# Kernel optimization log

Hardware: AMD Instinct MI355X
Metric: run time of the kernel (lower is better)

Reference implementation:

```python
import jax, jax.numpy as jnp
import numpy as np

N = 50000      # nodes
E = 800000     # edges
F_IN = 256     # num_n_feature
EMB = 128      # emb_size
GF = 32        # num_g_feature
G = 256        # graphs in batch
NEG_SLOPE = 0.2


def setup_inputs() -> dict:
    key = jax.random.key(0)
    ks = jax.random.split(key, 20)
    p = lambda i, shape: (jax.random.normal(ks[i], shape, jnp.float32) * 0.05)
    return {
        "x": jax.random.normal(ks[0], (N, F_IN), jnp.float32),
        "edges_idx": jax.random.randint(ks[1], (2, E), 0, N, dtype=jnp.int32),
        "batch_idx": jnp.sort(jax.random.randint(ks[2], (N,), 0, G, dtype=jnp.int32)),
        "g_features": jax.random.normal(ks[3], (G, GF), jnp.float32),
        # GATConv 1
        "W1": p(4, (F_IN, EMB)), "a1_src": p(5, (EMB,)), "a1_dst": p(6, (EMB,)), "b1": p(7, (EMB,)),
        # GATConv 2
        "W2": p(8, (EMB, EMB)), "a2_src": p(9, (EMB,)), "a2_dst": p(10, (EMB,)), "b2": p(11, (EMB,)),
        # lin_g
        "Wg": p(12, (GF, EMB)), "bg": p(13, (EMB,)),
        # out head: Linear(3*emb, 2)
        "Wo": p(14, (3 * EMB, 2)), "bo": p(15, (2,)),
    }


def gat_conv(x, src, dst, W, a_src, a_dst, b, n):
    """PyG GATConv, heads=1, with self-loops; attention dropout omitted (eval)."""
    h = x @ W                                  # [N, emb]
    loop = jnp.arange(n, dtype=src.dtype)
    src = jnp.concatenate([src, loop])         # add self loops
    dst = jnp.concatenate([dst, loop])
    e = jax.nn.leaky_relu((h @ a_src)[src] + (h @ a_dst)[dst], NEG_SLOPE)  # [E+N]
    # segment softmax over destination nodes
    m = jax.lax.stop_gradient(jax.ops.segment_max(e, dst, num_segments=n))
    m = jnp.where(jnp.isfinite(m), m, 0.0)
    p = jnp.exp(e - m[dst])
    den = jax.ops.segment_sum(p, dst, num_segments=n)
    alpha = p / den[dst]
    out = jax.ops.segment_sum(alpha[:, None] * h[src], dst, num_segments=n)
    return out + b


def reference(x, edges_idx, batch_idx, g_features,
              W1, a1_src, a1_dst, b1, W2, a2_src, a2_dst, b2,
              Wg, bg, Wo, bo):
    src, dst = edges_idx[0], edges_idx[1]
    h = gat_conv(x, src, dst, W1, a1_src, a1_dst, b1, N)
    h = gat_conv(h, src, dst, W2, a2_src, a2_dst, b2, N)
    # global mean / max pooling per graph
    counts = jax.ops.segment_sum(jnp.ones((N,), h.dtype), batch_idx, num_segments=G)
    mean = jax.ops.segment_sum(h, batch_idx, num_segments=G) / jnp.maximum(counts, 1.0)[:, None]
    mx = jax.ops.segment_max(h, batch_idx, num_segments=G)
    mx = jnp.where(jnp.isfinite(mx), mx, 0.0)
    g_ft = g_features @ Wg + bg
    flat = jnp.concatenate([mean, mx, g_ft], axis=1)   # [G, 3*emb]
    return jax.nn.log_softmax(flat @ Wo + bo, axis=-1)  # [G, 2]
```

## Files before the change

### kernel.cpp

```cpp
#include <hip/hip_runtime.h>
#include <hip/hip_bf16.h>

#define N_NODES 50000
#define N_EDGES 800000
#define FIN 256
#define EMB 128
#define NGRAPH 256
#define TOT_E (N_EDGES + N_NODES)
#define NP 98
#define RBLK 196
#define NB 391

typedef __bf16 bf16;
typedef __attribute__((ext_vector_type(8))) __bf16 bf16x8;
typedef __attribute__((ext_vector_type(4))) __bf16 bf16x4;
typedef __attribute__((ext_vector_type(2))) __bf16 bf16x2;
typedef __attribute__((ext_vector_type(4))) float f32x4;
typedef __attribute__((ext_vector_type(4))) int i32x4;

__global__ void transpose2_kernel(const float* __restrict__ W1, bf16* __restrict__ WT1,
                                  const float* __restrict__ W2, bf16* __restrict__ WT2) {
    int t = blockIdx.x * 256 + threadIdx.x;
    if (t < FIN * EMB) {
        int c = t / FIN, r = t - c * FIN;
        WT1[t] = (bf16)W1[r * EMB + c];
    } else if (t < FIN * EMB + EMB * EMB) {
        int u = t - FIN * EMB;
        int c = u / EMB, r = u - c * EMB;
        WT2[u] = (bf16)W2[r * EMB + c];
    }
}

__global__ __launch_bounds__(256)
void hist_part_kernel(const int* __restrict__ e_dst, int* __restrict__ counts,
                      int* __restrict__ mat) {
    __shared__ int lh[NP];
    int t = threadIdx.x;
    for (int k = t; k < NP; k += 256) lh[k] = 0;
    __syncthreads();
    const int NQ = N_EDGES / 4;
    int base = blockIdx.x * 1024;
#pragma unroll
    for (int j = 0; j < 4; ++j) {
        int i = base + j * 256 + t;
        if (i < NQ) {
            i32x4 d4 = *(const i32x4*)(e_dst + 4 * i);
#pragma unroll
            for (int k = 0; k < 4; ++k) {
                atomicAdd(&counts[d4[k]], 1);
                atomicAdd(&lh[d4[k] >> 9], 1);
            }
        }
    }
    __syncthreads();
    for (int k = t; k < NP; k += 256) mat[k * RBLK + blockIdx.x] = lh[k];
}

__global__ __launch_bounds__(1024)
void scan_block_kernel(const int* __restrict__ counts, int* __restrict__ offsets,
                       int* __restrict__ blocksums) {
    __shared__ int lds[1024];
    int t = threadIdx.x;
    int idx = blockIdx.x * 1024 + t;
    int v = (idx < N_NODES) ? counts[idx] + 1 : 0;
    lds[t] = v;
    __syncthreads();
    for (int d = 1; d < 1024; d <<= 1) {
        int u = (t >= d) ? lds[t - d] : 0;
        __syncthreads();
        lds[t] += u;
        __syncthreads();
    }
    if (idx < N_NODES) offsets[idx] = lds[t] - v;
    if (t == 1023) blocksums[blockIdx.x] = lds[1023];
}

__global__ __launch_bounds__(1024)
void scan_fix_kernel(int* __restrict__ offsets, const int* __restrict__ blocksums,
                     int nblk, int* __restrict__ sorted) {
    __shared__ int sprefix;
    int t = threadIdx.x, b = blockIdx.x;
    if (t < 64) {
        int v = (t < b && t < nblk) ? blocksums[t] : 0;
#pragma unroll
        for (int mk = 32; mk >= 1; mk >>= 1) v += __shfl_xor(v, mk);
        if (t == 0) sprefix = v;
    }
    __syncthreads();
    int idx = b * 1024 + t;
    if (idx < N_NODES) {
        int off = offsets[idx] + sprefix;
        offsets[idx] = off;
        sorted[off] = idx;
    }
    if (idx == 0) offsets[N_NODES] = TOT_E;
}

__global__ __launch_bounds__(256)
void rowscan_kernel(int* __restrict__ mat, int* __restrict__ rowsum) {
    __shared__ int lds[256];
    int p = blockIdx.x, t = threadIdx.x;
    int v = (t < RBLK) ? mat[p * RBLK + t] : 0;
    lds[t] = v;
    __syncthreads();
    for (int d = 1; d < 256; d <<= 1) {
        int u = (t >= d) ? lds[t - d] : 0;
        __syncthreads();
        lds[t] += u;
        __syncthreads();
    }
    if (t < RBLK) mat[p * RBLK + t] = lds[t] - v;
    if (t == 255) rowsum[p] = lds[255];
}

__global__ __launch_bounds__(128)
void partbase_kernel(const int* __restrict__ rowsum, int* __restrict__ poff) {
    __shared__ int lds[128];
    int t = threadIdx.x;
    int v = (t < NP) ? rowsum[t] : 0;
    lds[t] = v;
    __syncthreads();
    for (int d = 1; d < 128; d <<= 1) {
        int u = (t >= d) ? lds[t - d] : 0;
        __syncthreads();
        lds[t] += u;
        __syncthreads();
    }
    if (t < NP) poff[t] = lds[t] - v;
    if (t == 0) poff[NP] = N_EDGES;
}

__global__ __launch_bounds__(256)
void radix_scatter_kernel(const int* __restrict__ e_src, const int* __restrict__ e_dst,
                          const int* __restrict__ mat, const int* __restrict__ poff,
                          unsigned* __restrict__ pairs) {
    __shared__ int cur[NP];
    int t = threadIdx.x;
    for (int k = t; k < NP; k += 256) cur[k] = poff[k] + mat[k * RBLK + blockIdx.x];
    __syncthreads();
    const int NQ = N_EDGES / 4;
    int base = blockIdx.x * 1024;
#pragma unroll
    for (int j = 0; j < 4; ++j) {
        int i = base + j * 256 + t;
        if (i < NQ) {
            i32x4 d4 = *(const i32x4*)(e_dst + 4 * i);
            i32x4 s4 = *(const i32x4*)(e_src + 4 * i);
#pragma unroll
            for (int k = 0; k < 4; ++k) {
                int d = d4[k];
                int pos = atomicAdd(&cur[d >> 9], 1);
                pairs[pos] = ((unsigned)d << 16) | (unsigned)s4[k];
            }
        }
    }
}

__global__ __launch_bounds__(1024)
void bucket_place_kernel(const int* __restrict__ poff, const int* __restrict__ offsets,
                         const unsigned* __restrict__ pairs, int* __restrict__ sorted) {
    int b = blockIdx.x;
    int t = threadIdx.x;
    int lo = b * 128;
    __shared__ int cur[128];
    if (t < 128 && lo + t < N_NODES) cur[t] = offsets[lo + t] + 1;
    __syncthreads();
    int p = b >> 2;
    int p0 = poff[p], p1 = poff[p + 1];
    unsigned blo = (unsigned)b;
    for (int i = p0 + t; i < p1; i += 1024) {
        unsigned v = pairs[i];
        unsigned d = v >> 16;
        if ((d >> 7) == blo) {
            int pos = atomicAdd(&cur[d & 127], 1);
            sorted[pos] = (int)(v & 0xFFFFu);
        }
    }
}

template<int K, typename AT>
__global__ __launch_bounds__(256)
void gemm_kernel(const AT* __restrict__ A, const bf16* __restrict__ WT,
                 bf16* __restrict__ C, int M,
                 const float* __restrict__ a_src, const float* __restrict__ a_dst,
                 float* __restrict__ s_src, float* __restrict__ s_dst) {
    __shared__ __align__(16) bf16 As[32][64];
    __shared__ __align__(16) bf16 Bs[128][64];
    __shared__ float sbuf[2][32];
    int tid = threadIdx.x;
    int wave = tid >> 6, lane = tid & 63;
    int rowHalf = wave & 1, colHalf = wave >> 1;
    int m0 = blockIdx.x * 32;

    f32x4 acc[4];
#pragma unroll
    for (int i = 0; i < 4; ++i) acc[i] = (f32x4){0.f, 0.f, 0.f, 0.f};

    for (int k0 = 0; k0 < K; k0 += 64) {
        if constexpr (sizeof(AT) == 4) {
#pragma unroll
            for (int it = 0; it < 2; ++it) {
                int task = tid + it * 256;
                int row = task >> 4, seg4 = task & 15;
                int gr = m0 + row;
                float4 f = make_float4(0.f, 0.f, 0.f, 0.f);
                if (gr < M) f = *(const float4*)((const float*)A + (size_t)gr * K + k0 + seg4 * 4);
                bf16x4 b4 = (bf16x4){(bf16)f.x, (bf16)f.y, (bf16)f.z, (bf16)f.w};
                int slot = seg4 >> 1, half8 = seg4 & 1;
                int ss = slot ^ (row & 7);
                *(bf16x4*)(&As[row][ss * 8 + half8 * 4]) = b4;
            }
        } else {
            int row = tid >> 3, slot = tid & 7;
            int gr = m0 + row;
            uint4 v = make_uint4(0u, 0u, 0u, 0u);
            if (gr < M) v = *(const uint4*)((const bf16*)A + (size_t)gr * K + k0 + slot * 8);
            int ss = slot ^ (row & 7);
            *(uint4*)(&As[row][ss * 8]) = v;
        }
#pragma unroll
        for (int it = 0; it < 4; ++it) {
            int task = tid + it * 256;
            int col = task >> 3, slot = task & 7;
            uint4 v = *(const uint4*)(WT + (size_t)col * K + k0 + slot * 8);
            int ss = slot ^ (col & 7);
            *(uint4*)(&Bs[col][ss * 8]) = v;
        }
        __syncthreads();
        int tr = rowHalf * 16 + (lane & 15);
        int kseg = lane >> 4;
        bf16x8 af0 = *(const bf16x8*)(&As[tr][((kseg) ^ (tr & 7)) * 8]);
        bf16x8 af1 = *(const bf16x8*)(&As[tr][((4 + kseg) ^ (tr & 7)) * 8]);
#pragma unroll
        for (int n = 0; n < 4; ++n) {
            int c = colHalf * 64 + n * 16 + (lane & 15);
            bf16x8 b0 = *(const bf16x8*)(&Bs[c][((kseg) ^ (c & 7)) * 8]);
            bf16x8 b1 = *(const bf16x8*)(&Bs[c][((4 + kseg) ^ (c & 7)) * 8]);
            acc[n] = __builtin_amdgcn_mfma_f32_16x16x32_bf16(af0, b0, acc[n], 0, 0, 0);
            acc[n] = __builtin_amdgcn_mfma_f32_16x16x32_bf16(af1, b1, acc[n], 0, 0, 0);
        }
        __syncthreads();
    }
    int rbase = m0 + rowHalf * 16 + ((lane >> 4) << 2);
    int cb = lane & 15;
#pragma unroll
    for (int n = 0; n < 4; ++n) {
        int col = colHalf * 64 + n * 16 + cb;
#pragma unroll
        for (int rr = 0; rr < 4; ++rr) {
            int row = rbase + rr;
            if (row < M) C[(size_t)row * 128 + col] = (bf16)acc[n][rr];
        }
    }
    if (tid < 64) sbuf[tid >> 5][tid & 31] = 0.f;
    __syncthreads();
    float a_s[4], a_d[4];
#pragma unroll
    for (int n = 0; n < 4; ++n) {
        a_s[n] = a_src[colHalf * 64 + n * 16 + cb];
        a_d[n] = a_dst[colHalf * 64 + n * 16 + cb];
    }
#pragma unroll
    for (int rr = 0; rr < 4; ++rr) {
        float ps = 0.f, pd = 0.f;
#pragma unroll
        for (int n = 0; n < 4; ++n) {
            ps += acc[n][rr] * a_s[n];
            pd += acc[n][rr] * a_d[n];
        }
#pragma unroll
        for (int mk = 8; mk >= 1; mk >>= 1) {
            ps += __shfl_xor(ps, mk);
            pd += __shfl_xor(pd, mk);
        }
        if (cb == 0) {
            int tr16 = rowHalf * 16 + (lane >> 4) * 4 + rr;
            atomicAdd(&sbuf[0][tr16], ps);
            atomicAdd(&sbuf[1][tr16], pd);
        }
    }
    __syncthreads();
    if (tid < 32 && m0 + tid < M) {
        s_src[m0 + tid] = sbuf[0][tid];
        s_dst[m0 + tid] = sbuf[1][tid];
    }
}

template<typename OUT_T>
__global__ __launch_bounds__(256)
void agg_kernel(const int* __restrict__ offsets, const int* __restrict__ sorted_src,
                const float* __restrict__ s_src, const float* __restrict__ s_dst,
                const bf16* __restrict__ h, const float* __restrict__ bias,
                OUT_T* __restrict__ out) {
    int tid = threadIdx.x;
    int wave = tid >> 6, lane = tid & 63;
    int gl = lane & 15;
    int gbase = lane & 48;
    int d = blockIdx.x * 16 + wave * 4 + (lane >> 4);
    if (d >= N_NODES) return;
    int r0 = offsets[d];
    int deg = offsets[d + 1] - r0;
    float sd = s_dst[d];

    int sv0 = 0, sv1 = 0;
    float ev0 = -INFINITY, ev1 = -INFINITY;
    if (gl < deg) {
        sv0 = sorted_src[r0 + gl];
        float e = s_src[sv0] + sd;
        ev0 = (e > 0.f) ? e : 0.2f * e;
    }
    if (16 + gl < deg) {
        sv1 = sorted_src[r0 + 16 + gl];
        float e = s_src[sv1] + sd;
        ev1 = (e > 0.f) ? e : 0.2f * e;
    }
    float m = fmaxf(ev0, ev1);
    for (int i = 32 + gl; i < deg; i += 16) {
        int s = sorted_src[r0 + i];
        float e = s_src[s] + sd;
        e = (e > 0.f) ? e : 0.2f * e;
        m = fmaxf(m, e);
    }
#pragma unroll
    for (int mk = 8; mk >= 1; mk >>= 1) m = fmaxf(m, __shfl_xor(m, mk));

    float pv0 = (gl < deg) ? __expf(ev0 - m) : 0.f;
    float pv1 = (16 + gl < deg) ? __expf(ev1 - m) : 0.f;
    float den = pv0 + pv1;
    for (int i = 32 + gl; i < deg; i += 16) {
        int s = sorted_src[r0 + i];
        float e = s_src[s] + sd;
        e = (e > 0.f) ? e : 0.2f * e;
        den += __expf(e - m);
    }
#pragma unroll
    for (int mk = 8; mk >= 1; mk >>= 1) den += __shfl_xor(den, mk);

    float acc[8];
#pragma unroll
    for (int k = 0; k < 8; ++k) acc[k] = 0.f;

    int jm = (deg < 32) ? deg : 32;
#pragma unroll 8
    for (int j = 0; j < jm; ++j) {
        int src_lane = gbase + (j & 15);
        int s = __shfl((j < 16) ? sv0 : sv1, src_lane);
        float p = __shfl((j < 16) ? pv0 : pv1, src_lane);
        bf16x8 hv = *(const bf16x8*)(h + (size_t)s * 128 + gl * 8);
#pragma unroll
        for (int k = 0; k < 8; ++k) acc[k] += p * (float)hv[k];
    }
    for (int i = 32; i < deg; ++i) {
        int s = sorted_src[r0 + i];
        float e = s_src[s] + sd;
        e = (e > 0.f) ? e : 0.2f * e;
        float p = __expf(e - m);
        bf16x8 hv = *(const bf16x8*)(h + (size_t)s * 128 + gl * 8);
#pragma unroll
        for (int k = 0; k < 8; ++k) acc[k] += p * (float)hv[k];
    }

    float inv = 1.f / den;
    float4 bv0 = *(const float4*)(bias + gl * 8);
    float4 bv1 = *(const float4*)(bias + gl * 8 + 4);
    float o[8] = {acc[0] * inv + bv0.x, acc[1] * inv + bv0.y,
                  acc[2] * inv + bv0.z, acc[3] * inv + bv0.w,
                  acc[4] * inv + bv1.x, acc[5] * inv + bv1.y,
                  acc[6] * inv + bv1.z, acc[7] * inv + bv1.w};
    if constexpr (sizeof(OUT_T) == 2) {
        bf16x8 ov;
#pragma unroll
        for (int k = 0; k < 8; ++k) ov[k] = (bf16)o[k];
        *(bf16x8*)((bf16*)out + (size_t)d * 128 + gl * 8) = ov;
    } else {
        float* op = (float*)out + (size_t)d * 128 + gl * 8;
        *(float4*)op       = (float4){o[0], o[1], o[2], o[3]};
        *(float4*)(op + 4) = (float4){o[4], o[5], o[6], o[7]};
    }
}

__global__ __launch_bounds__(256)
void pool_kernel(const bf16* __restrict__ out2, const int* __restrict__ batch_idx,
                 float* __restrict__ mean, float* __restrict__ mx) {
    int g = blockIdx.x;
    int j = threadIdx.x & 127;
    int grp = threadIdx.x >> 7;
    int lo = 0, hi = N_NODES;
    while (lo < hi) { int mid = (lo + hi) >> 1; if (batch_idx[mid] < g) lo = mid + 1; else hi = mid; }
    int start = lo;
    hi = N_NODES;
    while (lo < hi) { int mid = (lo + hi) >> 1; if (batch_idx[mid] < g + 1) lo = mid + 1; else hi = mid; }
    int end = lo;

    float s = 0.f, mmax = -INFINITY;
    for (int r = start + grp; r < end; r += 2) {
        float v = (float)out2[(size_t)r * 128 + j];
        s += v;
        mmax = fmaxf(mmax, v);
    }
    __shared__ float ls[2][128], lm[2][128];
    ls[grp][j] = s; lm[grp][j] = mmax;
    __syncthreads();
    if (grp == 0) {
        int cnt = end - start;
        float sum = ls[0][j] + ls[1][j];
        float mv = fmaxf(lm[0][j], lm[1][j]);
        mean[g * 128 + j] = sum / fmaxf((float)cnt, 1.f);
        mx[g * 128 + j] = (cnt > 0) ? mv : 0.f;
    }
}

__global__ __launch_bounds__(128)
void head_kernel(const float* __restrict__ mean, const float* __restrict__ mx,
                 const float* __restrict__ gfeat, const float* __restrict__ Wg,
                 const float* __restrict__ bg, const float* __restrict__ Wo,
                 const float* __restrict__ bo, float* __restrict__ out) {
    int g = blockIdx.x;
    int j = threadIdx.x;
    float gft = bg[j];
#pragma unroll
    for (int k = 0; k < 32; ++k)
        gft += gfeat[g * 32 + k] * Wg[k * 128 + j];
    float mj = mean[g * 128 + j], xj = mx[g * 128 + j];
    float p0 = mj * Wo[j * 2 + 0] + xj * Wo[(128 + j) * 2 + 0] + gft * Wo[(256 + j) * 2 + 0];
    float p1 = mj * Wo[j * 2 + 1] + xj * Wo[(128 + j) * 2 + 1] + gft * Wo[(256 + j) * 2 + 1];
#pragma unroll
    for (int m = 32; m >= 1; m >>= 1) { p0 += __shfl_xor(p0, m); p1 += __shfl_xor(p1, m); }
    __shared__ float l0s[2], l1s[2];
    int wv = j >> 6;
    if ((j & 63) == 0) { l0s[wv] = p0; l1s[wv] = p1; }
    __syncthreads();
    if (j == 0) {
        float l0 = l0s[0] + l0s[1] + bo[0];
        float l1 = l1s[0] + l1s[1] + bo[1];
        float mm = fmaxf(l0, l1);
        float lse = mm + logf(__expf(l0 - mm) + __expf(l1 - mm));
        out[g * 2 + 0] = l0 - lse;
        out[g * 2 + 1] = l1 - lse;
    }
}

extern "C" void kernel_launch(void* const* d_in, const int* in_sizes, int n_in,
                              void* d_out, int out_size, void* d_ws, size_t ws_size,
                              hipStream_t stream) {
    const float* x     = (const float*)d_in[0];
    const int*   edges = (const int*)d_in[1];
    const int*   batch = (const int*)d_in[2];
    const float* gfeat = (const float*)d_in[3];
    const float* W1    = (const float*)d_in[4];
    const float* a1s   = (const float*)d_in[5];
    const float* a1d   = (const float*)d_in[6];
    const float* b1    = (const float*)d_in[7];
    const float* W2    = (const float*)d_in[8];
    const float* a2s   = (const float*)d_in[9];
    const float* a2d   = (const float*)d_in[10];
    const float* b2    = (const float*)d_in[11];
    const float* Wg    = (const float*)d_in[12];
    const float* bg    = (const float*)d_in[13];
    const float* Wo    = (const float*)d_in[14];
    const float* bo    = (const float*)d_in[15];

    char* ws = (char*)d_ws;
    bf16*     WT1       = (bf16*)(ws + 0);
    bf16*     WT2       = (bf16*)(ws + 65536);
    float*    s_src     = (float*)(ws + 98304);
    float*    s_dst     = (float*)(ws + 299008);
    int*      counts    = (int*)(ws + 499712);
    int*      blocksums = (int*)(ws + 700416);
    int*      mat       = (int*)(ws + 700672);
    int*      rowsum    = (int*)(ws + 777536);
    int*      poff      = (int*)(ws + 777984);
    int*      offsets   = (int*)(ws + 778432);
    int*      sorted    = (int*)(ws + 979136);
    bf16*     h         = (bf16*)(ws + 4502528);
    bf16*     out1      = (bf16*)(ws + 17302528);
    bf16*     out2      = (bf16*)(ws + 30102528);
    unsigned* pairs     = (unsigned*)(ws + 43002528);
    float*    pmean     = (float*)(ws + 55702528);
    float*    pmax      = (float*)(ws + 55833600);

    const int* e_src = edges;
    const int* e_dst = edges + N_EDGES;

    transpose2_kernel<<<(FIN * EMB + EMB * EMB + 255) / 256, 256, 0, stream>>>(W1, WT1, W2, WT2);

    hipMemsetAsync(counts, 0, N_NODES * sizeof(int), stream);
    hist_part_kernel<<<RBLK, 256, 0, stream>>>(e_dst, counts, mat);
    int nblk = (N_NODES + 1023) / 1024;
    scan_block_kernel<<<nblk, 1024, 0, stream>>>(counts, offsets, blocksums);
    scan_fix_kernel<<<nblk, 1024, 0, stream>>>(offsets, blocksums, nblk, sorted);
    rowscan_kernel<<<NP, 256, 0, stream>>>(mat, rowsum);
    partbase_kernel<<<1, 128, 0, stream>>>(rowsum, poff);
    radix_scatter_kernel<<<RBLK, 256, 0, stream>>>(e_src, e_dst, mat, poff, pairs);
    bucket_place_kernel<<<NB, 1024, 0, stream>>>(poff, offsets, pairs, sorted);

    int gemm_blocks = (N_NODES + 31) / 32;
    int agg_blocks = (N_NODES + 15) / 16;

    gemm_kernel<FIN, float><<<gemm_blocks, 256, 0, stream>>>(x, WT1, h, N_NODES,
                                                             a1s, a1d, s_src, s_dst);
    agg_kernel<bf16><<<agg_blocks, 256, 0, stream>>>(offsets, sorted, s_src, s_dst, h, b1, out1);

    gemm_kernel<EMB, bf16><<<gemm_blocks, 256, 0, stream>>>(out1, WT2, h, N_NODES,
                                                            a2s, a2d, s_src, s_dst);
    agg_kernel<bf16><<<agg_blocks, 256, 0, stream>>>(offsets, sorted, s_src, s_dst, h, b2, out2);

    pool_kernel<<<NGRAPH, 256, 0, stream>>>(out2, batch, pmean, pmax);
    head_kernel<<<NGRAPH, 128, 0, stream>>>(pmean, pmax, gfeat, Wg, bg, Wo, bo, (float*)d_out);
}
```

Baseline: 213.9 us.

## Fuse per-node counting and offset scan into per-partition CSR build kernel

Removes the global per-node atomic histogram, the memset and the two-pass global scan. Per-node counts and offsets are now computed inside each 512-node partition in LDS, then placed directly. The partition base is derived from poff plus nbase to account for the self-loop slots. This drops three launches and 800K global atomics, but uses only 98 blocks for the final placement instead of 391, so less parallelism.

```diff
diff --git a/kernel.cpp b/kernel.cpp
--- a/kernel.cpp
+++ b/kernel.cpp
@@ -9,7 +9,6 @@
 #define TOT_E (N_EDGES + N_NODES)
 #define NP 98
 #define RBLK 196
-#define NB 391
 
 typedef __bf16 bf16;
 typedef __attribute__((ext_vector_type(8))) __bf16 bf16x8;
@@ -31,9 +30,9 @@
     }
 }
 
-__global__ __launch_bounds__(256)
-void hist_part_kernel(const int* __restrict__ e_dst, int* __restrict__ counts,
-                      int* __restrict__ mat) {
+
+__global__ __launch_bounds__(256)
+void hist_part_kernel(const int* __restrict__ e_dst, int* __restrict__ mat) {
     __shared__ int lh[NP];
     int t = threadIdx.x;
     for (int k = t; k < NP; k += 256) lh[k] = 0;
@@ -46,54 +45,11 @@
         if (i < NQ) {
             i32x4 d4 = *(const i32x4*)(e_dst + 4 * i);
 #pragma unroll
-            for (int k = 0; k < 4; ++k) {
-                atomicAdd(&counts[d4[k]], 1);
-                atomicAdd(&lh[d4[k] >> 9], 1);
-            }
+            for (int k = 0; k < 4; ++k) atomicAdd(&lh[d4[k] >> 9], 1);
         }
     }
     __syncthreads();
     for (int k = t; k < NP; k += 256) mat[k * RBLK + blockIdx.x] = lh[k];
-}
-
-__global__ __launch_bounds__(1024)
-void scan_block_kernel(const int* __restrict__ counts, int* __restrict__ offsets,
-                       int* __restrict__ blocksums) {
-    __shared__ int lds[1024];
-    int t = threadIdx.x;
-    int idx = blockIdx.x * 1024 + t;
-    int v = (idx < N_NODES) ? counts[idx] + 1 : 0;
-    lds[t] = v;
-    __syncthreads();
-    for (int d = 1; d < 1024; d <<= 1) {
-        int u = (t >= d) ? lds[t - d] : 0;
-        __syncthreads();
-        lds[t] += u;
-        __syncthreads();
-    }
-    if (idx < N_NODES) offsets[idx] = lds[t] - v;
-    if (t == 1023) blocksums[blockIdx.x] = lds[1023];
-}
-
-__global__ __launch_bounds__(1024)
-void scan_fix_kernel(int* __restrict__ offsets, const int* __restrict__ blocksums,
-                     int nblk, int* __restrict__ sorted) {
-    __shared__ int sprefix;
-    int t = threadIdx.x, b = blockIdx.x;
-    if (t < 64) {
-        int v = (t < b && t < nblk) ? blocksums[t] : 0;
-#pragma unroll
-        for (int mk = 32; mk >= 1; mk >>= 1) v += __shfl_xor(v, mk);
-        if (t == 0) sprefix = v;
-    }
-    __syncthreads();
-    int idx = b * 1024 + t;
-    if (idx < N_NODES) {
-        int off = offsets[idx] + sprefix;
-        offsets[idx] = off;
-        sorted[off] = idx;
-    }
-    if (idx == 0) offsets[N_NODES] = TOT_E;
 }
 
 __global__ __launch_bounds__(256)
@@ -157,24 +113,41 @@
 }
 
 __global__ __launch_bounds__(1024)
-void bucket_place_kernel(const int* __restrict__ poff, const int* __restrict__ offsets,
-                         const unsigned* __restrict__ pairs, int* __restrict__ sorted) {
-    int b = blockIdx.x;
-    int t = threadIdx.x;
-    int lo = b * 128;
-    __shared__ int cur[128];
-    if (t < 128 && lo + t < N_NODES) cur[t] = offsets[lo + t] + 1;
-    __syncthreads();
-    int p = b >> 2;
+void part_build_kernel(const int* __restrict__ poff, const unsigned* __restrict__ pairs,
+                       int* __restrict__ offsets, int* __restrict__ sorted) {
+    int p = blockIdx.x, t = threadIdx.x;
+    int nbase = p * 512;
+    int valid = N_NODES - nbase;
+    valid = valid > 512 ? 512 : valid;
+    __shared__ int cnt[512], sc[512];
+    if (t < 512) cnt[t] = (t < valid) ? 1 : 0;
+    __syncthreads();
     int p0 = poff[p], p1 = poff[p + 1];
-    unsigned blo = (unsigned)b;
+    for (int i = p0 + t; i < p1; i += 1024)
+        atomicAdd(&cnt[(pairs[i] >> 16) & 511], 1);
+    __syncthreads();
+    int v = (t < 512) ? cnt[t] : 0;
+    if (t < 512) sc[t] = v;
+    __syncthreads();
+    for (int d = 1; d < 512; d <<= 1) {
+        int u = (t < 512 && t >= d) ? sc[t - d] : 0;
+        __syncthreads();
+        if (t < 512) sc[t] += u;
+        __syncthreads();
+    }
+    int base = p0 + nbase;
+    if (t < valid) {
+        int off = base + (sc[t] - v);
+        offsets[nbase + t] = off;
+        sorted[off] = nbase + t;
+        cnt[t] = off + 1;
+    }
+    if (p == 0 && t == 0) offsets[N_NODES] = TOT_E;
+    __syncthreads();
     for (int i = p0 + t; i < p1; i += 1024) {
-        unsigned v = pairs[i];
-        unsigned d = v >> 16;
-        if ((d >> 7) == blo) {
-            int pos = atomicAdd(&cur[d & 127], 1);
-            sorted[pos] = (int)(v & 0xFFFFu);
-        }
+        unsigned pr = pairs[i];
+        int pos = atomicAdd(&cnt[(pr >> 16) & 511], 1);
+        sorted[pos] = (int)(pr & 0xFFFFu);
     }
 }
 
@@ -465,8 +438,6 @@
     bf16*     WT2       = (bf16*)(ws + 65536);
     float*    s_src     = (float*)(ws + 98304);
     float*    s_dst     = (float*)(ws + 299008);
-    int*      counts    = (int*)(ws + 499712);
-    int*      blocksums = (int*)(ws + 700416);
     int*      mat       = (int*)(ws + 700672);
     int*      rowsum    = (int*)(ws + 777536);
     int*      poff      = (int*)(ws + 777984);
@@ -484,15 +455,11 @@
 
     transpose2_kernel<<<(FIN * EMB + EMB * EMB + 255) / 256, 256, 0, stream>>>(W1, WT1, W2, WT2);
 
-    hipMemsetAsync(counts, 0, N_NODES * sizeof(int), stream);
-    hist_part_kernel<<<RBLK, 256, 0, stream>>>(e_dst, counts, mat);
-    int nblk = (N_NODES + 1023) / 1024;
-    scan_block_kernel<<<nblk, 1024, 0, stream>>>(counts, offsets, blocksums);
-    scan_fix_kernel<<<nblk, 1024, 0, stream>>>(offsets, blocksums, nblk, sorted);
+    hist_part_kernel<<<RBLK, 256, 0, stream>>>(e_dst, mat);
     rowscan_kernel<<<NP, 256, 0, stream>>>(mat, rowsum);
     partbase_kernel<<<1, 128, 0, stream>>>(rowsum, poff);
     radix_scatter_kernel<<<RBLK, 256, 0, stream>>>(e_src, e_dst, mat, poff, pairs);
-    bucket_place_kernel<<<NB, 1024, 0, stream>>>(poff, offsets, pairs, sorted);
+    part_build_kernel<<<NP, 1024, 0, stream>>>(poff, pairs, offsets, sorted);
 
     int gemm_blocks = (N_NODES + 31) / 32;
     int agg_blocks = (N_NODES + 15) / 16;
```

Result: faster. 175.5 us (-18.0%).
